# Performance work log

Measured on AMD Instinct MI355X. Metric: run time of the kernel, lower is better.

## Reference

```python
import jax, jax.numpy as jnp
import numpy as np

# model geometry (matches init_kwargs cfg)
D = 768        # D_EMB
PATCH = 16
T = 8192
N = T // PATCH # 512 patch tokens
H = 12         # heads
HD = D // H    # 64 head dim
NL = 6         # layers
DFF = 4 * D
B = 8
LN_EPS = 1e-5


def setup_inputs() -> dict:
    key = jax.random.key(0)
    ks = iter(jax.random.split(key, 32))
    def g(shape, scale=0.02):
        return jax.random.normal(next(ks), shape, jnp.float32) * scale
    return dict(
        x=jax.random.normal(next(ks), (B, T), jnp.float32),
        pp_w=g((D, PATCH)), pp_b=jnp.zeros((D,), jnp.float32),
        pe=g((N, D)),
        ln1_g=jnp.ones((NL, D), jnp.float32), ln1_b=jnp.zeros((NL, D), jnp.float32),
        qkv_w=g((NL, 3 * D, D)), out_w=g((NL, D, D)),
        ln2_g=jnp.ones((NL, D), jnp.float32), ln2_b=jnp.zeros((NL, D), jnp.float32),
        fc1_w=g((NL, DFF, D)), fc2_w=g((NL, D, DFF)),
        lnf_g=jnp.ones((D,), jnp.float32), lnf_b=jnp.zeros((D,), jnp.float32),
        h1_w=g((D // 2, D)), h1_b=jnp.zeros((D // 2,), jnp.float32),
        h2_w=g((2, D // 2)), h2_b=jnp.zeros((2,), jnp.float32),
    )


def _ln(x, g, b):
    m = x.mean(-1, keepdims=True)
    v = ((x - m) ** 2).mean(-1, keepdims=True)
    return (x - m) / jnp.sqrt(v + LN_EPS) * g + b


def reference(x, pp_w, pp_b, pe, ln1_g, ln1_b, qkv_w, out_w,
              ln2_g, ln2_b, fc1_w, fc2_w, lnf_g, lnf_b,
              h1_w, h1_b, h2_w, h2_b):
    Bx = x.shape[0]
    # patch embed: [B, N, PATCH] @ W^T + b -> [B, N, D]
    z = jnp.einsum('bnp,dp->bnd', x[:, :N * PATCH].reshape(Bx, N, PATCH), pp_w) + pp_b
    z = z + pe  # positional embedding (arange indexes whole table)
    mask = jnp.tril(jnp.ones((N, N), dtype=bool))
    for i in range(NL):
        # --- attention (manual causal softmax, dropout=eval/no-op) ---
        h = _ln(z, ln1_g[i], ln1_b[i])
        qkv = jnp.einsum('bnd,ed->bne', h, qkv_w[i])            # [B,N,3D]
        qkv = qkv.reshape(Bx, N, 3, H, HD).transpose(2, 0, 3, 1, 4)
        q, k, v = qkv[0], qkv[1], qkv[2]                         # [B,H,N,HD]
        s = jnp.einsum('bhld,bhmd->bhlm', q, k) / np.sqrt(HD)
        s = jnp.where(mask, s, -jnp.inf)
        a = jax.nn.softmax(s, axis=-1)
        o = jnp.einsum('bhlm,bhmd->bhld', a, v)
        o = o.transpose(0, 2, 1, 3).reshape(Bx, N, D)
        z = z + jnp.einsum('bnd,ed->bne', o, out_w[i])
        # --- FFN (exact gelu, matching F.gelu default) ---
        h = _ln(z, ln2_g[i], ln2_b[i])
        f = jax.nn.gelu(jnp.einsum('bnd,fd->bnf', h, fc1_w[i]), approximate=False)
        z = z + jnp.einsum('bnf,df->bnd', f, fc2_w[i])
    enc = _ln(z, lnf_g, lnf_b).mean(axis=1)                      # [B, D]
    y = jax.nn.relu(enc @ h1_w.T + h1_b)
    return y @ h2_w.T + h2_b                                     # [B, 2]
```

## Files before the change

kernel.cpp:

```cpp
#include <hip/hip_runtime.h>
#include <hip/hip_bf16.h>
#include <math.h>

#define D_EMB 768
#define NPATCH 16
#define NTOK 512
#define NHEAD 12
#define HDIM 64
#define NLAYER 6
#define DFF 3072
#define BATCH 8
#define MTOK (BATCH * NTOK)

typedef __attribute__((ext_vector_type(8))) short bf16x8;
typedef __attribute__((ext_vector_type(4))) float f32x4;

__device__ __forceinline__ float bf2f(ushort s) {
    unsigned u = ((unsigned)s) << 16;
    return __builtin_bit_cast(float, u);
}
__device__ __forceinline__ ushort f2bf(float f) {
    unsigned u = __builtin_bit_cast(unsigned, f);
    unsigned r = (u + 0x7FFFu + ((u >> 16) & 1u)) >> 16;
    return (ushort)r;
}

__global__ __launch_bounds__(256)
void f2bf4_kernel(const float* __restrict__ s0, ushort* __restrict__ d0, int n0,
                  const float* __restrict__ s1, ushort* __restrict__ d1, int n1,
                  const float* __restrict__ s2, ushort* __restrict__ d2, int n2,
                  const float* __restrict__ s3, ushort* __restrict__ d3, int n3)
{
    int i = blockIdx.x * 256 + threadIdx.x;
    const float* s; ushort* d; int off;
    if (i < n0)                { s = s0; d = d0; off = i; }
    else if (i < n0 + n1)      { s = s1; d = d1; off = i - n0; }
    else if (i < n0 + n1 + n2) { s = s2; d = d2; off = i - n0 - n1; }
    else if (i < n0 + n1 + n2 + n3) { s = s3; d = d3; off = i - n0 - n1 - n2; }
    else return;
    float4 v = *(const float4*)(s + (size_t)off * 4);
    ushort4 o;
    o.x = f2bf(v.x); o.y = f2bf(v.y); o.z = f2bf(v.z); o.w = f2bf(v.w);
    *(ushort4*)(d + (size_t)off * 4) = o;
}

__global__ __launch_bounds__(256)
void patch_embed_kernel(const float* __restrict__ x, const float* __restrict__ pw,
                        const float* __restrict__ pb, const float* __restrict__ pe,
                        float* __restrict__ z)
{
    int bn = blockIdx.x;
    int b = bn >> 9, n = bn & 511;
    __shared__ float xs[NPATCH];
    int t = threadIdx.x;
    if (t < NPATCH) xs[t] = x[(size_t)b * 8192 + n * NPATCH + t];
    __syncthreads();
    for (int d = t; d < D_EMB; d += 256) {
        float acc = pb[d] + pe[(size_t)n * D_EMB + d];
        const float* w = pw + (size_t)d * NPATCH;
        #pragma unroll
        for (int p = 0; p < NPATCH; ++p) acc += xs[p] * w[p];
        z[(size_t)bn * D_EMB + d] = acc;
    }
}

__device__ __forceinline__ float block_reduce_sum_256(float v)
{
    __shared__ float lds[4];
    #pragma unroll
    for (int o = 32; o > 0; o >>= 1) v += __shfl_xor(v, o);
    int lane = threadIdx.x & 63, wid = threadIdx.x >> 6;
    __syncthreads();
    if (lane == 0) lds[wid] = v;
    __syncthreads();
    return lds[0] + lds[1] + lds[2] + lds[3];
}

__device__ __forceinline__ void store_val(float* p, float v)  { *p = v; }
__device__ __forceinline__ void store_val(ushort* p, float v) { *p = f2bf(v); }

template<typename OT>
__global__ __launch_bounds__(256)
void ln_kernel(const float* __restrict__ x, const float* __restrict__ g,
               const float* __restrict__ bta, OT* __restrict__ y)
{
    int row = blockIdx.x;
    const float* xr = x + (size_t)row * D_EMB;
    int t = threadIdx.x;
    float vals[3];
    float s = 0.f;
    #pragma unroll
    for (int i = 0; i < 3; ++i) { vals[i] = xr[t + i * 256]; s += vals[i]; }
    float mean = block_reduce_sum_256(s) * (1.0f / D_EMB);
    float ss = 0.f;
    #pragma unroll
    for (int i = 0; i < 3; ++i) { float d = vals[i] - mean; ss += d * d; }
    float var = block_reduce_sum_256(ss) * (1.0f / D_EMB);
    float rstd = rsqrtf(var + 1e-5f);
    #pragma unroll
    for (int i = 0; i < 3; ++i) {
        int d = t + i * 256;
        store_val(y + (size_t)row * D_EMB + d, (vals[i] - mean) * rstd * g[d] + bta[d]);
    }
}

template<int EPI, typename OT, bool SPLITK>
__global__ __launch_bounds__(256)
void mfma_gemm(const ushort* __restrict__ A,
               const ushort* __restrict__ W,
               OT* __restrict__ C,
               const float* __restrict__ res,
               int N, int K, int lda)
{
    __shared__ ushort As[64 * 64];
    __shared__ ushort Bs[128 * 64];

    int gx = gridDim.x, gy = gridDim.y, gz = SPLITK ? gridDim.z : 1;
    int total = gx * gy * gz;
    int bx = blockIdx.x, by = blockIdx.y;
    int bz = SPLITK ? blockIdx.z : 0;
    if ((total & 7) == 0) {
        int flat = bx + gx * (by + gy * bz);
        int q = total >> 3;
        int logical = (flat & 7) * q + (flat >> 3);
        by = logical % gy;
        int rem = logical / gy;
        bx = rem % gx;
        bz = rem / gx;
    }
    int bm = by * 64, bn = bx * 128;

    const ushort* Ab = A + (size_t)bz * K;
    const ushort* Wb = W + (size_t)bz * K;
    OT* Cb = C;

    int tid = threadIdx.x;
    int w = tid >> 6, l = tid & 63;
    int lr = l & 15, lg = l >> 4;
    f32x4 acc[4][2] = {};

    int srow = w * 8 + (l >> 3);
    int pcol = l & 7;

    for (int k0 = 0; k0 < K; k0 += 64) {
        #pragma unroll
        for (int j = 0; j < 2; ++j) {
            int row = j * 32 + srow;
            int lcol = pcol ^ (row & 7);
            const ushort* sa = Ab + (size_t)(bm + row) * lda + k0 + (lcol << 3);
            __builtin_amdgcn_global_load_lds(
                (const __attribute__((address_space(1))) unsigned int*)sa,
                (__attribute__((address_space(3))) unsigned int*)&As[row * 64 + (pcol << 3)],
                16, 0, 0);
        }
        #pragma unroll
        for (int j = 0; j < 4; ++j) {
            int row = j * 32 + srow;
            int lcol = pcol ^ (row & 7);
            const ushort* sb = Wb + (size_t)(bn + row) * lda + k0 + (lcol << 3);
            __builtin_amdgcn_global_load_lds(
                (const __attribute__((address_space(1))) unsigned int*)sb,
                (__attribute__((address_space(3))) unsigned int*)&Bs[row * 64 + (pcol << 3)],
                16, 0, 0);
        }
        __syncthreads();

        #pragma unroll
        for (int kk = 0; kk < 64; kk += 32) {
            int c = (kk >> 3) + lg;
            bf16x8 a[4], b[2];
            #pragma unroll
            for (int m = 0; m < 4; ++m) {
                int row = m * 16 + lr;
                a[m] = *(const bf16x8*)(&As[row * 64 + ((c ^ (row & 7)) << 3)]);
            }
            #pragma unroll
            for (int n = 0; n < 2; ++n) {
                int row = w * 32 + n * 16 + lr;
                b[n] = *(const bf16x8*)(&Bs[row * 64 + ((c ^ (row & 7)) << 3)]);
            }
            #pragma unroll
            for (int m = 0; m < 4; ++m)
                #pragma unroll
                for (int n = 0; n < 2; ++n)
                    acc[m][n] = __builtin_amdgcn_mfma_f32_16x16x32_bf16(a[m], b[n], acc[m][n], 0, 0, 0);
        }
        __syncthreads();
    }

    int r0 = lg * 4;
    #pragma unroll
    for (int m = 0; m < 4; ++m) {
        #pragma unroll
        for (int n = 0; n < 2; ++n) {
            #pragma unroll
            for (int j = 0; j < 4; ++j) {
                int gm = bm + m * 16 + r0 + j;
                int gn = bn + w * 32 + n * 16 + lr;
                float v = acc[m][n][j];
                if (EPI == 1) v = 0.5f * v * (1.0f + erff(v * 0.70710678118654752f));
                if (EPI == 2) v += res[(size_t)gm * N + gn];
                if (EPI == 3) {
                    atomicAdd((float*)&Cb[(size_t)gm * N + gn], v);
                } else {
                    store_val(Cb + (size_t)gm * N + gn, v);
                }
            }
        }
    }
}

__global__ __launch_bounds__(256)
void attn_mfma_kernel(const ushort* __restrict__ qkv, ushort* __restrict__ o)
{
    int w = threadIdx.x >> 6, l = threadIdx.x & 63;
    int qt = blockIdx.x * 4 + w;
    int h = blockIdx.y, b = blockIdx.z;
    int q0 = qt * 16;
    int lr = l & 15, lg = l >> 4;

    const size_t rs = 3 * D_EMB;
    const ushort* qbase = qkv + ((size_t)(b * NTOK)) * rs + h * HDIM;
    const ushort* kbase = qbase + D_EMB;
    const ushort* vbase = qbase + 2 * D_EMB;

    bf16x8 qf[2];
    qf[0] = *(const bf16x8*)(qbase + (size_t)(q0 + lr) * rs + lg * 8);
    qf[1] = *(const bf16x8*)(qbase + (size_t)(q0 + lr) * rs + 32 + lg * 8);

    f32x4 oacc[4] = {};
    float m_j[4], l_j[4];
    #pragma unroll
    for (int j = 0; j < 4; ++j) { m_j[j] = -1e30f; l_j[j] = 0.f; }

    __shared__ ushort P_lds[4][16][40];

    int ntiles = q0 / 32 + 1;
    for (int mt = 0; mt < ntiles; ++mt) {
        int m0 = mt * 32;
        f32x4 s[2] = {};
        #pragma unroll
        for (int kb = 0; kb < 2; ++kb) {
            const ushort* kr = kbase + (size_t)(m0 + kb * 16 + lr) * rs;
            bf16x8 k0 = *(const bf16x8*)(kr + lg * 8);
            bf16x8 k1 = *(const bf16x8*)(kr + 32 + lg * 8);
            s[kb] = __builtin_amdgcn_mfma_f32_16x16x32_bf16(qf[0], k0, s[kb], 0, 0, 0);
            s[kb] = __builtin_amdgcn_mfma_f32_16x16x32_bf16(qf[1], k1, s[kb], 0, 0, 0);
        }
        bool partial = (m0 + 31 > q0);
        float p[2][4], mx[4];
        #pragma unroll
        for (int j = 0; j < 4; ++j) {
            int qr = q0 + lg * 4 + j;
            float s0 = s[0][j] * 0.125f;
            float s1 = s[1][j] * 0.125f;
            if (partial) {
                if (m0 + lr > qr)      s0 = -1e30f;
                if (m0 + 16 + lr > qr) s1 = -1e30f;
            }
            p[0][j] = s0; p[1][j] = s1;
            float mm = fmaxf(s0, s1);
            mm = fmaxf(mm, __shfl_xor(mm, 1));
            mm = fmaxf(mm, __shfl_xor(mm, 2));
            mm = fmaxf(mm, __shfl_xor(mm, 4));
            mm = fmaxf(mm, __shfl_xor(mm, 8));
            mx[j] = mm;
        }
        #pragma unroll
        for (int j = 0; j < 4; ++j) {
            float mnew = fmaxf(m_j[j], mx[j]);
            float scale = __expf(m_j[j] - mnew);
            float p0 = __expf(p[0][j] - mnew);
            float p1 = __expf(p[1][j] - mnew);
            p[0][j] = p0; p[1][j] = p1;
            float rsum = p0 + p1;
            rsum += __shfl_xor(rsum, 1);
            rsum += __shfl_xor(rsum, 2);
            rsum += __shfl_xor(rsum, 4);
            rsum += __shfl_xor(rsum, 8);
            l_j[j] = l_j[j] * scale + rsum;
            m_j[j] = mnew;
            #pragma unroll
            for (int i = 0; i < 4; ++i) oacc[i][j] *= scale;
        }
        #pragma unroll
        for (int kb = 0; kb < 2; ++kb)
            #pragma unroll
            for (int j = 0; j < 4; ++j)
                P_lds[w][lg * 4 + j][kb * 16 + lr] = f2bf(p[kb][j]);
        asm volatile("s_waitcnt lgkmcnt(0)" ::: "memory");
        bf16x8 pa = *(const bf16x8*)(&P_lds[w][lr][lg * 8]);
        #pragma unroll
        for (int i = 0; i < 4; ++i) {
            bf16x8 vf;
            const ushort* vp = vbase + (size_t)(m0 + lg * 8) * rs + i * 16 + lr;
            #pragma unroll
            for (int j = 0; j < 8; ++j) vf[j] = (short)vp[(size_t)j * rs];
            oacc[i] = __builtin_amdgcn_mfma_f32_16x16x32_bf16(pa, vf, oacc[i], 0, 0, 0);
        }
    }
    #pragma unroll
    for (int i = 0; i < 4; ++i) {
        #pragma unroll
        for (int j = 0; j < 4; ++j) {
            int qr = q0 + lg * 4 + j;
            int d  = i * 16 + lr;
            float v = oacc[i][j] / l_j[j];
            o[((size_t)(b * NTOK + qr)) * D_EMB + h * HDIM + d] = f2bf(v);
        }
    }
}

__global__ void mean_kernel(const float* __restrict__ x, float* __restrict__ enc)
{
    int b = blockIdx.x; int d = threadIdx.x;
    float s = 0.f;
    for (int n = 0; n < NTOK; ++n) s += x[((size_t)(b * NTOK + n)) * D_EMB + d];
    enc[b * D_EMB + d] = s * (1.0f / NTOK);
}

__global__ void head1_kernel(const float* __restrict__ enc, const float* __restrict__ w,
                             const float* __restrict__ bias, float* __restrict__ r)
{
    int b = blockIdx.x; int j = threadIdx.x;
    float acc = bias[j];
    const float* e = enc + b * D_EMB;
    const float* wr = w + (size_t)j * D_EMB;
    for (int k = 0; k < D_EMB; ++k) acc += e[k] * wr[k];
    r[b * 384 + j] = fmaxf(acc, 0.f);
}

__global__ void head2_kernel(const float* __restrict__ r, const float* __restrict__ w,
                             const float* __restrict__ bias, float* __restrict__ out)
{
    int idx = threadIdx.x;
    if (idx >= 16) return;
    int b = idx >> 1, j = idx & 1;
    float acc = bias[j];
    for (int k = 0; k < 384; ++k) acc += r[b * 384 + k] * w[j * 384 + k];
    out[b * 2 + j] = acc;
}

extern "C" void kernel_launch(void* const* d_in, const int* in_sizes, int n_in,
                              void* d_out, int out_size, void* d_ws, size_t ws_size,
                              hipStream_t stream)
{
    const float* x     = (const float*)d_in[0];
    const float* pp_w  = (const float*)d_in[1];
    const float* pp_b  = (const float*)d_in[2];
    const float* pe    = (const float*)d_in[3];
    const float* ln1_g = (const float*)d_in[4];
    const float* ln1_b = (const float*)d_in[5];
    const float* qkv_w = (const float*)d_in[6];
    const float* out_w = (const float*)d_in[7];
    const float* ln2_g = (const float*)d_in[8];
    const float* ln2_b = (const float*)d_in[9];
    const float* fc1_w = (const float*)d_in[10];
    const float* fc2_w = (const float*)d_in[11];
    const float* lnf_g = (const float*)d_in[12];
    const float* lnf_b = (const float*)d_in[13];
    const float* h1_w  = (const float*)d_in[14];
    const float* h1_b  = (const float*)d_in[15];
    const float* h2_w  = (const float*)d_in[16];
    const float* h2_b  = (const float*)d_in[17];
    float* out = (float*)d_out;

    char* p = (char*)d_ws;
    float*  z      = (float*)p;  p += (size_t)MTOK * D_EMB * 4;
    ushort* big_bf = (ushort*)p; p += (size_t)MTOK * DFF * 2;
    ushort* h_bf   = (ushort*)p; p += (size_t)MTOK * D_EMB * 2;
    ushort* wq_bf  = (ushort*)p; p += (size_t)3 * D_EMB * D_EMB * 2;
    ushort* wo_bf  = (ushort*)p; p += (size_t)D_EMB * D_EMB * 2;
    ushort* wf1_bf = (ushort*)p; p += (size_t)DFF * D_EMB * 2;
    ushort* wf2_bf = (ushort*)p; p += (size_t)D_EMB * DFF * 2;
    float*  enc    = (float*)p;  p += BATCH * D_EMB * 4;
    float*  r1     = (float*)p;  p += BATCH * 384 * 4;
    float*  lnf_out = (float*)big_bf;

    patch_embed_kernel<<<MTOK, 256, 0, stream>>>(x, pp_w, pp_b, pe, z);

    const int nq = 3 * D_EMB * D_EMB, no = D_EMB * D_EMB, nf = DFF * D_EMB;
    const int n4q = nq / 4, n4o = no / 4, n4f = nf / 4;
    const int cvt_blocks = (n4q + n4o + 2 * n4f + 255) / 256;

    for (int i = 0; i < NLAYER; ++i) {
        f2bf4_kernel<<<cvt_blocks, 256, 0, stream>>>(
            qkv_w + (size_t)i * nq, wq_bf,  n4q,
            out_w + (size_t)i * no, wo_bf,  n4o,
            fc1_w + (size_t)i * nf, wf1_bf, n4f,
            fc2_w + (size_t)i * nf, wf2_bf, n4f);

        ln_kernel<ushort><<<MTOK, 256, 0, stream>>>(z, ln1_g + i * D_EMB, ln1_b + i * D_EMB, h_bf);

        dim3 gq((3 * D_EMB) / 128, MTOK / 64);
        mfma_gemm<0, ushort, false><<<gq, 256, 0, stream>>>(h_bf, wq_bf, big_bf, nullptr,
                                                            3 * D_EMB, D_EMB, D_EMB);

        dim3 ga(NTOK / 64, NHEAD, BATCH);
        attn_mfma_kernel<<<ga, 256, 0, stream>>>(big_bf, h_bf);

        dim3 gp(D_EMB / 128, MTOK / 64);
        mfma_gemm<2, float, false><<<gp, 256, 0, stream>>>(h_bf, wo_bf, z, z,
                                                           D_EMB, D_EMB, D_EMB);

        ln_kernel<ushort><<<MTOK, 256, 0, stream>>>(z, ln2_g + i * D_EMB, ln2_b + i * D_EMB, h_bf);

        dim3 g1(DFF / 128, MTOK / 64);
        mfma_gemm<1, ushort, false><<<g1, 256, 0, stream>>>(h_bf, wf1_bf, big_bf, nullptr,
                                                            DFF, D_EMB, D_EMB);

        dim3 g2(D_EMB / 128, MTOK / 64, 2);
        mfma_gemm<3, float, true><<<g2, 256, 0, stream>>>(big_bf, wf2_bf, z, nullptr,
                                                          D_EMB, DFF / 2, DFF);
    }

    ln_kernel<float><<<MTOK, 256, 0, stream>>>(z, lnf_g, lnf_b, lnf_out);
    mean_kernel<<<BATCH, D_EMB, 0, stream>>>(lnf_out, enc);
    head1_kernel<<<BATCH, 384, 0, stream>>>(enc, h1_w, h1_b, r1);
    head2_kernel<<<1, 64, 0, stream>>>(r1, h2_w, h2_b, out);
}
```

Measured before the change: 1.175 ms.

## Enlarge GEMM tiles to 128x128 with 2x2 warp layout and split-K out-projection

The MFMA GEMM tile grows from 64x128 to 128x128, and each of the four waves now computes a 64x64 sub-tile laid out 2x2, so every LDS fragment is reused across more MFMAs. The XCD-aware block remapping is rewritten to group M-rows per XCD, and grids are halved in M. The output projection becomes a 2-way split-K launch that adds into z with atomics instead of a residual epilogue. The intent is higher arithmetic intensity and fewer blocks; the costs are more accumulator registers (lower occupancy), fewer blocks to fill the GPU, and atomic traffic on the projection.

```diff
diff --git a/kernel.cpp b/kernel.cpp
--- a/kernel.cpp
+++ b/kernel.cpp
@@ -112,23 +112,22 @@
                const float* __restrict__ res,
                int N, int K, int lda)
 {
-    __shared__ ushort As[64 * 64];
+    __shared__ ushort As[128 * 64];
     __shared__ ushort Bs[128 * 64];
 
-    int gx = gridDim.x, gy = gridDim.y, gz = SPLITK ? gridDim.z : 1;
-    int total = gx * gy * gz;
+    int gx = gridDim.x, gy = gridDim.y;
     int bx = blockIdx.x, by = blockIdx.y;
     int bz = SPLITK ? blockIdx.z : 0;
-    if ((total & 7) == 0) {
+    if ((gy & 7) == 0) {
         int flat = bx + gx * (by + gy * bz);
-        int q = total >> 3;
-        int logical = (flat & 7) * q + (flat >> 3);
-        by = logical % gy;
-        int rem = logical / gy;
+        int xcd = flat & 7, j = flat >> 3;
+        int ry = gy >> 3;
+        by = xcd * ry + (j % ry);
+        int rem = j / ry;
         bx = rem % gx;
         bz = rem / gx;
     }
-    int bm = by * 64, bn = bx * 128;
+    int bm = by * 128, bn = bx * 128;
 
     const ushort* Ab = A + (size_t)bz * K;
     const ushort* Wb = W + (size_t)bz * K;
@@ -136,28 +135,24 @@
 
     int tid = threadIdx.x;
     int w = tid >> 6, l = tid & 63;
+    int wr = w >> 1, wc = w & 1;
     int lr = l & 15, lg = l >> 4;
-    f32x4 acc[4][2] = {};
-
-    int srow = w * 8 + (l >> 3);
+    f32x4 acc[4][4] = {};
+
+    int srow = w * 32 + (l >> 3);
     int pcol = l & 7;
 
     for (int k0 = 0; k0 < K; k0 += 64) {
         #pragma unroll
-        for (int j = 0; j < 2; ++j) {
-            int row = j * 32 + srow;
+        for (int j = 0; j < 4; ++j) {
+            int row = srow + j * 8;
             int lcol = pcol ^ (row & 7);
             const ushort* sa = Ab + (size_t)(bm + row) * lda + k0 + (lcol << 3);
+            const ushort* sb = Wb + (size_t)(bn + row) * lda + k0 + (lcol << 3);
             __builtin_amdgcn_global_load_lds(
                 (const __attribute__((address_space(1))) unsigned int*)sa,
                 (__attribute__((address_space(3))) unsigned int*)&As[row * 64 + (pcol << 3)],
                 16, 0, 0);
-        }
-        #pragma unroll
-        for (int j = 0; j < 4; ++j) {
-            int row = j * 32 + srow;
-            int lcol = pcol ^ (row & 7);
-            const ushort* sb = Wb + (size_t)(bn + row) * lda + k0 + (lcol << 3);
             __builtin_amdgcn_global_load_lds(
                 (const __attribute__((address_space(1))) unsigned int*)sb,
                 (__attribute__((address_space(3))) unsigned int*)&Bs[row * 64 + (pcol << 3)],
@@ -168,21 +163,21 @@
         #pragma unroll
         for (int kk = 0; kk < 64; kk += 32) {
             int c = (kk >> 3) + lg;
-            bf16x8 a[4], b[2];
+            bf16x8 a[4], b[4];
             #pragma unroll
             for (int m = 0; m < 4; ++m) {
-                int row = m * 16 + lr;
+                int row = wr * 64 + m * 16 + lr;
                 a[m] = *(const bf16x8*)(&As[row * 64 + ((c ^ (row & 7)) << 3)]);
             }
             #pragma unroll
-            for (int n = 0; n < 2; ++n) {
-                int row = w * 32 + n * 16 + lr;
+            for (int n = 0; n < 4; ++n) {
+                int row = wc * 64 + n * 16 + lr;
                 b[n] = *(const bf16x8*)(&Bs[row * 64 + ((c ^ (row & 7)) << 3)]);
             }
             #pragma unroll
             for (int m = 0; m < 4; ++m)
                 #pragma unroll
-                for (int n = 0; n < 2; ++n)
+                for (int n = 0; n < 4; ++n)
                     acc[m][n] = __builtin_amdgcn_mfma_f32_16x16x32_bf16(a[m], b[n], acc[m][n], 0, 0, 0);
         }
         __syncthreads();
@@ -192,11 +187,11 @@
     #pragma unroll
     for (int m = 0; m < 4; ++m) {
         #pragma unroll
-        for (int n = 0; n < 2; ++n) {
+        for (int n = 0; n < 4; ++n) {
             #pragma unroll
             for (int j = 0; j < 4; ++j) {
-                int gm = bm + m * 16 + r0 + j;
-                int gn = bn + w * 32 + n * 16 + lr;
+                int gm = bm + wr * 64 + m * 16 + r0 + j;
+                int gn = bn + wc * 64 + n * 16 + lr;
                 float v = acc[m][n][j];
                 if (EPI == 1) v = 0.5f * v * (1.0f + erff(v * 0.70710678118654752f));
                 if (EPI == 2) v += res[(size_t)gm * N + gn];
@@ -392,24 +387,24 @@
 
         ln_kernel<ushort><<<MTOK, 256, 0, stream>>>(z, ln1_g + i * D_EMB, ln1_b + i * D_EMB, h_bf);
 
-        dim3 gq((3 * D_EMB) / 128, MTOK / 64);
+        dim3 gq((3 * D_EMB) / 128, MTOK / 128);
         mfma_gemm<0, ushort, false><<<gq, 256, 0, stream>>>(h_bf, wq_bf, big_bf, nullptr,
                                                             3 * D_EMB, D_EMB, D_EMB);
 
         dim3 ga(NTOK / 64, NHEAD, BATCH);
         attn_mfma_kernel<<<ga, 256, 0, stream>>>(big_bf, h_bf);
 
-        dim3 gp(D_EMB / 128, MTOK / 64);
-        mfma_gemm<2, float, false><<<gp, 256, 0, stream>>>(h_bf, wo_bf, z, z,
-                                                           D_EMB, D_EMB, D_EMB);
+        dim3 gp(D_EMB / 128, MTOK / 128, 2);
+        mfma_gemm<3, float, true><<<gp, 256, 0, stream>>>(h_bf, wo_bf, z, nullptr,
+                                                          D_EMB, D_EMB / 2, D_EMB);
 
         ln_kernel<ushort><<<MTOK, 256, 0, stream>>>(z, ln2_g + i * D_EMB, ln2_b + i * D_EMB, h_bf);
 
-        dim3 g1(DFF / 128, MTOK / 64);
+        dim3 g1(DFF / 128, MTOK / 128);
         mfma_gemm<1, ushort, false><<<g1, 256, 0, stream>>>(h_bf, wf1_bf, big_bf, nullptr,
                                                             DFF, D_EMB, D_EMB);
 
-        dim3 g2(D_EMB / 128, MTOK / 64, 2);
+        dim3 g2(D_EMB / 128, MTOK / 128, 2);
         mfma_gemm<3, float, true><<<g2, 256, 0, stream>>>(big_bf, wf2_bf, z, nullptr,
                                                           D_EMB, DFF / 2, DFF);
     }
```

After: 1.225 ms. 1.04x slower.
